# Kernel optimization log

Measured on AMD Instinct MI355X. Metric: run time of the kernel, lower is better.

Reference implementation:

```python
import jax, jax.numpy as jnp
import numpy as np

B, S, R = 32, 1024, 1024
HID, OUT = 512, 1024

def setup_inputs() -> dict:
    key = jax.random.key(0)
    k1, k2, k3, k4, k5, k6 = jax.random.split(key, 6)
    return {
        "representation": jax.random.normal(k1, (B, 1, R), dtype=jnp.float32),
        "size_matrix": jax.random.uniform(k2, (B, S, 1), dtype=jnp.float32),
        "W1": jax.random.normal(k3, (HID, R), dtype=jnp.float32) * 0.02,
        "b1": jax.random.normal(k4, (HID,), dtype=jnp.float32) * 0.02,
        "W2": jax.random.normal(k5, (OUT, HID), dtype=jnp.float32) * 0.02,
        "b2": jax.random.normal(k6, (OUT,), dtype=jnp.float32) * 0.02,
    }

def reference(representation, size_matrix, W1, b1, W2, b2):
    # bmm(ones_like(size_matrix)[B,S,1], representation[B,1,R]) == broadcast to [B,S,R]
    ones = jnp.ones_like(size_matrix)                       # [B,S,1]
    sized = jnp.einsum('bso,bor->bsr', ones, representation)  # [B,S,R]
    # per-position 2-layer MLP, fused into two batched GEMMs over all B*S positions
    h = jax.nn.relu(jnp.einsum('bsr,hr->bsh', sized, W1) + b1)  # [B,S,HID]
    out = jnp.einsum('bsh,oh->bso', h, W2) + b2                 # [B,S,OUT]
    return out
```

## Files before the change

### kernel.cpp

```cpp
#include <hip/hip_runtime.h>
#include <hip/hip_bf16.h>

#define BB   32
#define SS   1024
#define RR   1024
#define HID  512
#define OUTD 1024

__global__ __launch_bounds__(64) void layer1_kernel(
    const float* __restrict__ rep, const float* __restrict__ W1,
    const float* __restrict__ b1, float* __restrict__ h) {
  const int lane = threadIdx.x;
  const int g    = lane >> 4;
  const int l16  = lane & 15;
  const int jq   = blockIdx.x >> 3;
  const int b0   = (blockIdx.x & 7) << 2;
  const int j    = (jq << 2) + g;

  const float4* w4 = reinterpret_cast<const float4*>(W1 + (size_t)j * RR);
  const float4* r0 = reinterpret_cast<const float4*>(rep + (size_t)b0 * RR);
  const float4* r1 = reinterpret_cast<const float4*>(rep + (size_t)(b0 + 1) * RR);
  const float4* r2 = reinterpret_cast<const float4*>(rep + (size_t)(b0 + 2) * RR);
  const float4* r3 = reinterpret_cast<const float4*>(rep + (size_t)(b0 + 3) * RR);
  float a0 = 0.f, a1 = 0.f, a2 = 0.f, a3 = 0.f;
#pragma unroll
  for (int t = 0; t < 16; ++t) {
    const int idx = l16 + 16 * t;
    const float4 w = w4[idx];
    const float4 x0 = r0[idx];
    const float4 x1 = r1[idx];
    const float4 x2 = r2[idx];
    const float4 x3 = r3[idx];
    a0 += w.x * x0.x + w.y * x0.y + w.z * x0.z + w.w * x0.w;
    a1 += w.x * x1.x + w.y * x1.y + w.z * x1.z + w.w * x1.w;
    a2 += w.x * x2.x + w.y * x2.y + w.z * x2.z + w.w * x2.w;
    a3 += w.x * x3.x + w.y * x3.y + w.z * x3.z + w.w * x3.w;
  }
#pragma unroll
  for (int m = 1; m <= 8; m <<= 1) {
    a0 += __shfl_xor(a0, m);
    a1 += __shfl_xor(a1, m);
    a2 += __shfl_xor(a2, m);
    a3 += __shfl_xor(a3, m);
  }
  if (l16 == 0) {
    const float bb = b1[j];
    h[(size_t)b0 * HID + j]       = fmaxf(a0 + bb, 0.f);
    h[(size_t)(b0 + 1) * HID + j] = fmaxf(a1 + bb, 0.f);
    h[(size_t)(b0 + 2) * HID + j] = fmaxf(a2 + bb, 0.f);
    h[(size_t)(b0 + 3) * HID + j] = fmaxf(a3 + bb, 0.f);
  }
}

__global__ __launch_bounds__(64) void layer2_kernel(
    const float* __restrict__ h, const float* __restrict__ W2,
    const float* __restrict__ b2, float* __restrict__ out) {
  const int lane = threadIdx.x;
  const int g    = lane >> 4;
  const int l16  = lane & 15;
  const int kq   = blockIdx.x >> 3;
  const int b0   = (blockIdx.x & 7) << 2;
  const int k    = (kq << 2) + g;

  const float4* w4 = reinterpret_cast<const float4*>(W2 + (size_t)k * HID);
  const float4* h0 = reinterpret_cast<const float4*>(h + (size_t)b0 * HID);
  const float4* h1 = reinterpret_cast<const float4*>(h + (size_t)(b0 + 1) * HID);
  const float4* h2 = reinterpret_cast<const float4*>(h + (size_t)(b0 + 2) * HID);
  const float4* h3 = reinterpret_cast<const float4*>(h + (size_t)(b0 + 3) * HID);
  float a0 = 0.f, a1 = 0.f, a2 = 0.f, a3 = 0.f;
#pragma unroll
  for (int t = 0; t < 8; ++t) {
    const int idx = l16 + 16 * t;
    const float4 w = w4[idx];
    const float4 x0 = h0[idx];
    const float4 x1 = h1[idx];
    const float4 x2 = h2[idx];
    const float4 x3 = h3[idx];
    a0 += w.x * x0.x + w.y * x0.y + w.z * x0.z + w.w * x0.w;
    a1 += w.x * x1.x + w.y * x1.y + w.z * x1.z + w.w * x1.w;
    a2 += w.x * x2.x + w.y * x2.y + w.z * x2.z + w.w * x2.w;
    a3 += w.x * x3.x + w.y * x3.y + w.z * x3.z + w.w * x3.w;
  }
#pragma unroll
  for (int m = 1; m <= 8; m <<= 1) {
    a0 += __shfl_xor(a0, m);
    a1 += __shfl_xor(a1, m);
    a2 += __shfl_xor(a2, m);
    a3 += __shfl_xor(a3, m);
  }
  if (l16 == 0) {
    const float bb = b2[k];
    out[(size_t)b0 * SS * OUTD + k]       = a0 + bb;
    out[(size_t)(b0 + 1) * SS * OUTD + k] = a1 + bb;
    out[(size_t)(b0 + 2) * SS * OUTD + k] = a2 + bb;
    out[(size_t)(b0 + 3) * SS * OUTD + k] = a3 + bb;
  }
}

__global__ __launch_bounds__(256) void bcast_kernel(float* __restrict__ out) {
  const int b  = blockIdx.x >> 7;
  const int sc = blockIdx.x & 127;
  float4* __restrict__ base =
      reinterpret_cast<float4*>(out) + (size_t)b * SS * (OUTD / 4);
  const float4 v = base[threadIdx.x];
  const int s0 = sc << 3;
#pragma unroll
  for (int i = 0; i < 8; ++i) {
    const int s = s0 + i;
    if (s != 0) base[(size_t)s * (OUTD / 4) + threadIdx.x] = v;
  }
}

extern "C" void kernel_launch(void* const* d_in, const int* in_sizes, int n_in,
                              void* d_out, int out_size, void* d_ws, size_t ws_size,
                              hipStream_t stream) {
  const float* rep = (const float*)d_in[0];
  const float* W1 = (const float*)d_in[2];
  const float* b1 = (const float*)d_in[3];
  const float* W2 = (const float*)d_in[4];
  const float* b2 = (const float*)d_in[5];
  float* out = (float*)d_out;
  float* h   = (float*)d_ws;

  layer1_kernel<<<1024, 64, 0, stream>>>(rep, W1, b1, h);
  layer2_kernel<<<2048, 64, 0, stream>>>(h, W2, b2, out);
  bcast_kernel<<<BB * 128, 256, 0, stream>>>(out);
}
```

Before: 35.54 us.

## Fuse layer-2 GEMV with broadcast store into one kernel

Merges the layer-2 matvec and the broadcast kernel into a single kernel. Each block computes a 128-wide output chunk for one batch into shared memory, then writes that chunk to 256 sequence rows. This drops one launch and the read-back of row 0 that the broadcast previously did. In exchange, each output chunk is recomputed by 4 blocks (one per sequence quarter), which adds redundant W2 reads.

```diff
diff --git a/kernel.cpp b/kernel.cpp
--- a/kernel.cpp
+++ b/kernel.cpp
@@ -52,62 +52,49 @@
   }
 }
 
-__global__ __launch_bounds__(64) void layer2_kernel(
+__global__ __launch_bounds__(256) void l2bcast_kernel(
     const float* __restrict__ h, const float* __restrict__ W2,
     const float* __restrict__ b2, float* __restrict__ out) {
-  const int lane = threadIdx.x;
-  const int g    = lane >> 4;
-  const int l16  = lane & 15;
-  const int kq   = blockIdx.x >> 3;
-  const int b0   = (blockIdx.x & 7) << 2;
-  const int k    = (kq << 2) + g;
+  __shared__ float s_h[HID];
+  __shared__ float s_o[128];
+  const int tid = threadIdx.x;
+  const int b   = blockIdx.x >> 5;
+  const int kc  = (blockIdx.x >> 2) & 7;
+  const int sc  = blockIdx.x & 3;
+  const int k0  = kc << 7;
 
-  const float4* w4 = reinterpret_cast<const float4*>(W2 + (size_t)k * HID);
-  const float4* h0 = reinterpret_cast<const float4*>(h + (size_t)b0 * HID);
-  const float4* h1 = reinterpret_cast<const float4*>(h + (size_t)(b0 + 1) * HID);
-  const float4* h2 = reinterpret_cast<const float4*>(h + (size_t)(b0 + 2) * HID);
-  const float4* h3 = reinterpret_cast<const float4*>(h + (size_t)(b0 + 3) * HID);
-  float a0 = 0.f, a1 = 0.f, a2 = 0.f, a3 = 0.f;
-#pragma unroll
-  for (int t = 0; t < 8; ++t) {
-    const int idx = l16 + 16 * t;
-    const float4 w = w4[idx];
-    const float4 x0 = h0[idx];
-    const float4 x1 = h1[idx];
-    const float4 x2 = h2[idx];
-    const float4 x3 = h3[idx];
-    a0 += w.x * x0.x + w.y * x0.y + w.z * x0.z + w.w * x0.w;
-    a1 += w.x * x1.x + w.y * x1.y + w.z * x1.z + w.w * x1.w;
-    a2 += w.x * x2.x + w.y * x2.y + w.z * x2.z + w.w * x2.w;
-    a3 += w.x * x3.x + w.y * x3.y + w.z * x3.z + w.w * x3.w;
-  }
-#pragma unroll
-  for (int m = 1; m <= 8; m <<= 1) {
-    a0 += __shfl_xor(a0, m);
-    a1 += __shfl_xor(a1, m);
-    a2 += __shfl_xor(a2, m);
-    a3 += __shfl_xor(a3, m);
-  }
-  if (l16 == 0) {
-    const float bb = b2[k];
-    out[(size_t)b0 * SS * OUTD + k]       = a0 + bb;
-    out[(size_t)(b0 + 1) * SS * OUTD + k] = a1 + bb;
-    out[(size_t)(b0 + 2) * SS * OUTD + k] = a2 + bb;
-    out[(size_t)(b0 + 3) * SS * OUTD + k] = a3 + bb;
-  }
-}
+  reinterpret_cast<float2*>(s_h)[tid] =
+      reinterpret_cast<const float2*>(h + (size_t)b * HID)[tid];
+  __syncthreads();
 
-__global__ __launch_bounds__(256) void bcast_kernel(float* __restrict__ out) {
-  const int b  = blockIdx.x >> 7;
-  const int sc = blockIdx.x & 127;
-  float4* __restrict__ base =
-      reinterpret_cast<float4*>(out) + (size_t)b * SS * (OUTD / 4);
-  const float4 v = base[threadIdx.x];
-  const int s0 = sc << 3;
+  const int gg  = tid >> 4;
+  const int l16 = tid & 15;
+  const float4* s_h4 = reinterpret_cast<const float4*>(s_h);
 #pragma unroll
   for (int i = 0; i < 8; ++i) {
-    const int s = s0 + i;
-    if (s != 0) base[(size_t)s * (OUTD / 4) + threadIdx.x] = v;
+    const int k = k0 + (i << 4) + gg;
+    const float4* w = reinterpret_cast<const float4*>(W2 + (size_t)k * HID);
+    float acc = 0.f;
+#pragma unroll
+    for (int t = 0; t < 8; ++t) {
+      const float4 wv = w[l16 + 16 * t];
+      const float4 xv = s_h4[l16 + 16 * t];
+      acc += wv.x * xv.x + wv.y * xv.y + wv.z * xv.z + wv.w * xv.w;
+    }
+#pragma unroll
+    for (int m = 1; m <= 8; m <<= 1) acc += __shfl_xor(acc, m);
+    if (l16 == 0) s_o[(i << 4) + gg] = acc + b2[k];
+  }
+  __syncthreads();
+
+  const float4 v = reinterpret_cast<const float4*>(s_o)[tid & 31];
+  const int r0 = (sc << 8) + (tid >> 5);
+  const size_t base4 = (((size_t)b * SS * OUTD) + (size_t)k0) >> 2;
+  float4* __restrict__ o4 = reinterpret_cast<float4*>(out);
+#pragma unroll
+  for (int p = 0; p < 32; ++p) {
+    const int s = r0 + (p << 3);
+    o4[base4 + (size_t)s * (OUTD / 4) + (tid & 31)] = v;
   }
 }
 
@@ -123,6 +110,5 @@
   float* h   = (float*)d_ws;
 
   layer1_kernel<<<1024, 64, 0, stream>>>(rep, W1, b1, h);
-  layer2_kernel<<<2048, 64, 0, stream>>>(h, W2, b2, out);
-  bcast_kernel<<<BB * 128, 256, 0, stream>>>(out);
+  l2bcast_kernel<<<1024, 256, 0, stream>>>(h, W2, b2, out);
 }
```

Measured after the change: 39.65 us. 1.12x slower.
